# Performance work log

Measured on AMD Instinct MI355X. Metric: run time of the kernel, lower is better.

Reference implementation:

```python
import jax, jax.numpy as jnp
import numpy as np

B, S, D = 2, 2048, 2048
H, HKV = 16, 4
GROUPS = H // HKV
RQ, RKV = 1024, 512
DH, DR = 192, 64          # q_head_dim, rope dim
DN = DH - DR              # nrope dim = 128
DV = 128                  # v head dim
EPS = 1e-20


def setup_inputs() -> dict:
    key = jax.random.key(0)
    ks = jax.random.split(key, 8)
    inp = {
        "hidden_states": jax.random.normal(ks[0], (B, S, D), jnp.float32),
        # causal mask (0 = masked), as used by masked_fill(mask == 0, -inf)
        "attention_mask": jnp.tril(jnp.ones((S, S), jnp.int32))[None, None],
        "w_qa": jax.random.normal(ks[1], (D, RQ), jnp.float32) * 0.02,
        "b_qa": jnp.zeros((RQ,), jnp.float32),
        "g_q": jnp.ones((RQ,), jnp.float32),
        "w_qb": jax.random.normal(ks[2], (RQ, H * DH), jnp.float32) * 0.02,
        "b_qb": jnp.zeros((H * DH,), jnp.float32),
        "w_kva": jax.random.normal(ks[3], (D, RKV + DR), jnp.float32) * 0.02,
        "b_kva": jnp.zeros((RKV + DR,), jnp.float32),
        "g_kv": jnp.ones((RKV,), jnp.float32),
        "w_kvb": jax.random.normal(ks[4], (RKV, HKV * (DN + DV)), jnp.float32) * 0.02,
        "b_kvb": jnp.zeros((HKV * (DN + DV),), jnp.float32),
        "w_o": jax.random.normal(ks[5], (H * DV, D), jnp.float32) * 0.02,
        "b_o": jnp.zeros((D,), jnp.float32),
    }
    return inp


def _rmsnorm(x, g, eps=EPS):
    var = jnp.mean(x * x, axis=-1, keepdims=True)
    return x * jax.lax.rsqrt(var + eps) * g


def _rope_cos_sin(seq_len, dim, base=10000.0, dtype=jnp.float32):
    inv_freq = 1.0 / (base ** (jnp.arange(0, dim, 2, dtype=jnp.float32) / dim))
    t = jnp.arange(seq_len, dtype=jnp.float32)
    freqs = jnp.outer(t, inv_freq)                    # [S, dim/2]
    emb = jnp.concatenate([freqs, freqs], axis=-1)    # [S, dim]
    return jnp.cos(emb).astype(dtype), jnp.sin(emb).astype(dtype)


def _apply_rope(x, cos, sin):
    # x: [..., S, dr]; rotate_half convention
    d2 = x.shape[-1] // 2
    x1, x2 = x[..., :d2], x[..., d2:]
    rot = jnp.concatenate([-x2, x1], axis=-1)
    return x * cos + rot * sin


def reference(hidden_states, attention_mask, w_qa, b_qa, g_q, w_qb, b_qb,
              w_kva, b_kva, g_kv, w_kvb, b_kvb, w_o, b_o):
    b, s, _ = hidden_states.shape
    # --- Q: LoRA down -> RMSNorm -> LoRA up ---
    q_a = hidden_states @ w_qa + b_qa                         # [B,S,RQ]
    q_b = _rmsnorm(q_a, g_q) @ w_qb + b_qb                    # [B,S,H*DH]
    q_b = q_b.reshape(b, s, H, DH).transpose(0, 2, 1, 3)      # [B,H,S,DH]
    q_nrope, q_rope = q_b[..., :DN], q_b[..., DN:]
    # --- KV: LoRA down, split latent / shared rope key ---
    kv_a = hidden_states @ w_kva + b_kva                      # [B,S,RKV+DR]
    kv_c, k_rope = kv_a[..., :RKV], kv_a[..., RKV:]
    kv_b = _rmsnorm(kv_c, g_kv) @ w_kvb + b_kvb               # [B,S,HKV*(DN+DV)]
    kv_b = kv_b.reshape(b, s, HKV, DN + DV).transpose(0, 2, 1, 3)
    k_nrope, value_states = kv_b[..., :DN], kv_b[..., DN:]    # [B,HKV,S,DN/DV]
    # --- split RoPE ---
    cos, sin = _rope_cos_sin(s, DR, dtype=hidden_states.dtype)
    q_rope = _apply_rope(q_rope, cos, sin)                    # [B,H,S,DR]
    k_rope = _apply_rope(k_rope[:, None], cos, sin)           # [B,1,S,DR]
    # --- assemble heads (rope part first, matching source concat order) ---
    query_states = jnp.concatenate([q_rope, q_nrope], axis=-1)            # [B,H,S,DH]
    key_states = jnp.concatenate(
        [jnp.broadcast_to(k_rope, (b, HKV, s, DR)), k_nrope], axis=-1)    # [B,HKV,S,DH]
    # --- GQA expand kv heads ---
    key_states = jnp.repeat(key_states, GROUPS, axis=1)                   # [B,H,S,DH]
    value_states = jnp.repeat(value_states, GROUPS, axis=1)               # [B,H,S,DV]
    # --- attention ---
    scores = jnp.einsum('bhqd,bhkd->bhqk', query_states, key_states)
    scores = scores / jnp.sqrt(jnp.asarray(DH, scores.dtype))
    scores = jnp.where(attention_mask == 0, jnp.asarray(-1e9, scores.dtype), scores)
    weights = jax.nn.softmax(scores, axis=-1)
    attn_out = jnp.einsum('bhqk,bhkd->bhqd', weights, value_states)       # [B,H,S,DV]
    attn_out = attn_out.transpose(0, 2, 1, 3).reshape(b, s, H * DV)
    return attn_out @ w_o + b_o
```

## Files before the change

kernel.cpp:

```cpp
#include <hip/hip_runtime.h>
#include <hip/hip_bf16.h>
#include <stdint.h>

#define DEV static __device__ __forceinline__

typedef __attribute__((ext_vector_type(8))) short bf16x8;
typedef __attribute__((ext_vector_type(4))) float f32x4;
typedef __attribute__((ext_vector_type(16))) float f32x16;

constexpr int Bc = 2, Sc = 2048, Dc = 2048;
constexpr int Hc = 16, HKVc = 4;
constexpr int RQc = 1024, RKVc = 512;
constexpr int DHc = 192, DRc = 64, DVc = 128;

DEV unsigned short f2bf(float f) {
  union { float f; uint32_t u; } v; v.f = f;
  uint32_t r = v.u + 0x7FFFu + ((v.u >> 16) & 1u);
  return (unsigned short)(r >> 16);
}
DEV float bf2f(unsigned short u) {
  union { uint32_t u; float f; } v; v.u = ((uint32_t)u) << 16;
  return v.f;
}

DEV void gload_lds16(const unsigned short* g, unsigned short* l) {
  __builtin_amdgcn_global_load_lds(
      (const __attribute__((address_space(1))) unsigned int*)g,
      (__attribute__((address_space(3))) unsigned int*)l, 16, 0, 0);
}

__global__ void f2b_kernel(const float* __restrict__ in, unsigned short* __restrict__ out, int n) {
  int stride = gridDim.x * blockDim.x;
  for (int i = blockIdx.x * blockDim.x + threadIdx.x; i * 4 < n; i += stride) {
    float4 v = reinterpret_cast<const float4*>(in)[i];
    union { unsigned short u[4]; uint64_t q; } pk;
    pk.u[0] = f2bf(v.x); pk.u[1] = f2bf(v.y); pk.u[2] = f2bf(v.z); pk.u[3] = f2bf(v.w);
    reinterpret_cast<uint64_t*>(out)[i] = pk.q;
  }
}

__global__ void wtrans_kernel(const float* __restrict__ in, unsigned short* __restrict__ out,
                              int R, int C) {
  __shared__ float tile[32][33];
  const int c0 = blockIdx.x * 32, r0 = blockIdx.y * 32;
  const int tx = threadIdx.x & 31, ty = threadIdx.x >> 5;
#pragma unroll
  for (int i = 0; i < 32; i += 8)
    tile[ty + i][tx] = in[(size_t)(r0 + ty + i) * C + c0 + tx];
  __syncthreads();
#pragma unroll
  for (int i = 0; i < 32; i += 8)
    out[(size_t)(c0 + ty + i) * R + r0 + tx] = f2bf(tile[tx][ty + i]);
}

__global__ void rope_table_kernel(float* __restrict__ cosT, float* __restrict__ sinT) {
  int idx = blockIdx.x * blockDim.x + threadIdx.x;
  if (idx >= Sc * DRc) return;
  int t = idx >> 6;
  int j = idx & 63;
  float inv = exp2f(-13.287712379549449f * (float)(j & 31) * (1.0f / 32.0f));
  float f = (float)t * inv;
  cosT[idx] = cosf(f);
  sinT[idx] = sinf(f);
}

template<int R>
__global__ void rmsnorm_kernel(const float* __restrict__ in, int istride,
                               const float* __restrict__ g, unsigned short* __restrict__ out) {
  int row = blockIdx.x;
  const float* x = in + (size_t)row * istride;
  float ss = 0.f;
  for (int j = threadIdx.x; j < R; j += 256) { float v = x[j]; ss += v * v; }
  for (int off = 32; off; off >>= 1) ss += __shfl_down(ss, off, 64);
  __shared__ float wsum[4];
  if ((threadIdx.x & 63) == 0) wsum[threadIdx.x >> 6] = ss;
  __syncthreads();
  float tot = wsum[0] + wsum[1] + wsum[2] + wsum[3];
  float rs = rsqrtf(tot * (1.0f / R) + 1e-20f);
  for (int j = threadIdx.x; j < R; j += 256)
    out[(size_t)row * R + j] = f2bf(x[j] * rs * g[j]);
}

template<bool OUT_BF16, bool NG>
__global__ __launch_bounds__(256)
void gemm_tn_kernel(const unsigned short* __restrict__ A, const unsigned short* __restrict__ Bt,
                    const float* __restrict__ bias, void* __restrict__ Cout,
                    int M, int N, int K) {
  __shared__ __align__(16) unsigned short As[2][128 * 64];
  __shared__ __align__(16) unsigned short Bs[2][128 * 64];
  const int t = threadIdx.x, lane = t & 63, wave = t >> 6;
  const int wm = wave >> 1, wn = wave & 1;
  const int m0 = blockIdx.x * 128, n0 = blockIdx.y * 128;
  const int fr = lane & 15, fo = (lane >> 4) * 8, rg = lane >> 4;
  const int srow = lane >> 3;
  const int scol = (lane & 7) * 8;

  const unsigned short* Ap[4];
  const unsigned short* Bp[4];
#pragma unroll
  for (int i = 0; i < 4; ++i) {
    const int ar = m0 + wave * 32 + i * 8 + srow;
    Ap[i] = A + (size_t)ar * K + scol;
    int br = n0 + wave * 32 + i * 8 + srow;
    if (NG) br = br < N ? br : N - 1;
    Bp[i] = Bt + (size_t)br * K + scol;
  }

  auto stage = [&](int buf, int k0) {
#pragma unroll
    for (int i = 0; i < 4; ++i) {
      gload_lds16(Ap[i] + k0, &As[buf][(wave * 32 + i * 8) * 64]);
      gload_lds16(Bp[i] + k0, &Bs[buf][(wave * 32 + i * 8) * 64]);
    }
  };

  f32x4 acc[4][4] = {};
  const int nt = K >> 6;

  stage(0, 0);
  for (int tt = 0; tt < nt; ++tt) {
    const int cur = tt & 1;
    if (tt + 1 < nt) {
      stage(cur ^ 1, (tt + 1) * 64);
      asm volatile("s_waitcnt vmcnt(8)" ::: "memory");
    } else {
      asm volatile("s_waitcnt vmcnt(0)" ::: "memory");
    }
    __syncthreads();
#pragma unroll
    for (int kk = 0; kk < 64; kk += 32) {
      bf16x8 af[4], bf[4];
#pragma unroll
      for (int m = 0; m < 4; ++m)
        af[m] = *reinterpret_cast<const bf16x8*>(&As[cur][(wm * 64 + m * 16 + fr) * 64 + kk + fo]);
#pragma unroll
      for (int n = 0; n < 4; ++n)
        bf[n] = *reinterpret_cast<const bf16x8*>(&Bs[cur][(wn * 64 + n * 16 + fr) * 64 + kk + fo]);
      __builtin_amdgcn_s_setprio(1);
#pragma unroll
      for (int m = 0; m < 4; ++m)
#pragma unroll
        for (int n = 0; n < 4; ++n)
          acc[m][n] = __builtin_amdgcn_mfma_f32_16x16x32_bf16(af[m], bf[n], acc[m][n], 0, 0, 0);
      __builtin_amdgcn_s_setprio(0);
    }
    __syncthreads();
  }

#pragma unroll
  for (int m = 0; m < 4; ++m) {
    const int row = m0 + wm * 64 + m * 16 + rg * 4;
#pragma unroll
    for (int n = 0; n < 4; ++n) {
      const int col = n0 + wn * 64 + n * 16 + fr;
      if (NG && col >= N) continue;
      const float bb = bias[col];
#pragma unroll
      for (int r = 0; r < 4; ++r) {
        float v = acc[m][n][r] + bb;
        if (OUT_BF16)
          reinterpret_cast<unsigned short*>(Cout)[(size_t)(row + r) * N + col] = f2bf(v);
        else
          reinterpret_cast<float*>(Cout)[(size_t)(row + r) * N + col] = v;
      }
    }
  }
}

__global__ void prep_q_kernel(const unsigned short* __restrict__ qb,
                              const float* __restrict__ cosT, const float* __restrict__ sinT,
                              unsigned short* __restrict__ Q) {
  const float QS = 0.07216878364870323f * 1.4426950408889634f;
  int bs = blockIdx.x;
  int s = bs & (Sc - 1);
  int b = bs >> 11;
  int d = threadIdx.x;
  if (d >= 192) return;
  for (int h = 0; h < Hc; ++h) {
    const unsigned short* src = qb + (size_t)bs * (Hc * DHc) + h * DHc;
    float v;
    if (d < 128) {
      v = bf2f(src[d]);
    } else {
      int j = d - 128;
      float x = bf2f(src[128 + j]);
      float other = bf2f(src[128 + (j < 32 ? j + 32 : j - 32)]);
      float c = cosT[s * 64 + j], sn = sinT[s * 64 + j];
      v = (j < 32) ? (x * c - other * sn) : (x * c + other * sn);
    }
    Q[(((size_t)(b * Hc + h)) * Sc + s) * DHc + d] = f2bf(v * QS);
  }
}

__global__ void prep_k_kernel(const unsigned short* __restrict__ kvb,
                              const float* __restrict__ ccat,
                              const float* __restrict__ cosT, const float* __restrict__ sinT,
                              unsigned short* __restrict__ K) {
  int bs = blockIdx.x;
  int s = bs & (Sc - 1);
  int b = bs >> 11;
  int d = threadIdx.x;
  if (d >= 192) return;
  unsigned short ropeval = 0;
  if (d >= 128) {
    int j = d - 128;
    float x = ccat[(size_t)bs * 1600 + 1536 + j];
    float other = ccat[(size_t)bs * 1600 + 1536 + (j < 32 ? j + 32 : j - 32)];
    float c = cosT[s * 64 + j], sn = sinT[s * 64 + j];
    float v = (j < 32) ? (x * c - other * sn) : (x * c + other * sn);
    ropeval = f2bf(v);
  }
  const size_t off = (size_t)(s >> 6) * 12288 + (d >> 3) * 512 + (s & 63) * 8 + (d & 7);
  for (int kvh = 0; kvh < HKVc; ++kvh) {
    unsigned short o;
    if (d < 128) o = kvb[(size_t)bs * 1024 + kvh * 256 + d];
    else o = ropeval;
    K[(size_t)(b * HKVc + kvh) * Sc * DHc + off] = o;
  }
}

__global__ void vtrans_kernel(const unsigned short* __restrict__ kvb, unsigned short* __restrict__ Vt) {
  int idx = blockIdx.x;
  int dt = idx & 3;  idx >>= 2;
  int st = idx & 63; idx >>= 6;
  int kvh = idx & 3; idx >>= 2;
  int b = idx;
  __shared__ unsigned short tile[32][33];
  int t = threadIdx.x;
  int c = t & 31, r0 = t >> 5;
#pragma unroll
  for (int i = 0; i < 4; ++i) {
    int r = r0 + i * 8;
    int s = st * 32 + r;
    tile[r][c] = kvb[((size_t)(b * Sc + s)) * 1024 + kvh * 256 + 128 + dt * 32 + c];
  }
  __syncthreads();
#pragma unroll
  for (int i = 0; i < 4; ++i) {
    int r = r0 + i * 8;
    const int dd = dt * 32 + r;
    const int k = st * 32 + c;
    const size_t pos = (size_t)(k >> 6) * 8192 + ((k >> 3) & 7) * 1024 + dd * 8 + (k & 7);
    Vt[(size_t)((b * HKVc + kvh)) * DVc * Sc + pos] = tile[c][r];
  }
}

__global__ __launch_bounds__(128)
void attn_kernel(const unsigned short* __restrict__ Q, const unsigned short* __restrict__ Kt,
                 const unsigned short* __restrict__ Vt, unsigned short* __restrict__ attnOut) {
  __shared__ __align__(16) unsigned short Ks[2][12288];

  const int bid = blockIdx.x;
  const int g = bid & 7;
  const int b = g >> 2, kvh = g & 3;
  const int r2 = bid >> 3;
  const int hp = r2 & 1;
  const int u = r2 >> 1;
  const int w = threadIdx.x >> 6;
  const int h = kvh * 4 + hp * 2 + w;
  const int lane = threadIdx.x & 63;
  const int l31 = lane & 31, hi = lane >> 5;

  const unsigned short* Qh = Q + (size_t)(b * Hc + h) * Sc * DHc;
  const unsigned short* Kg = Kt + (size_t)(b * HKVc + kvh) * Sc * DHc;
  const unsigned short* Vg = Vt + (size_t)(b * HKVc + kvh) * DVc * Sc;

  auto stage = [&](int buf, int t) {
    const unsigned short* Kb = Kg + (size_t)t * 12288;
#pragma unroll
    for (int i = 0; i < 12; ++i) {
      const int ii = w * 12 + i;
      gload_lds16(Kb + ii * 512 + lane * 8, &Ks[buf][ii * 512]);
    }
  };

#pragma unroll 1
  for (int pan = 0; pan < 2; ++pan) {
    const int sub = pan ? u : (63 - u);
    const int q0 = sub * 32;
    const int q = q0 + l31;
    const int NT = (sub >> 1) + 1;

    bf16x8 qf[12];
#pragma unroll
    for (int f = 0; f < 12; ++f)
      qf[f] = *reinterpret_cast<const bf16x8*>(Qh + (size_t)q * DHc + f * 16 + hi * 8);

    f32x16 ot[4] = {};
    float m = -INFINITY, lsum = 0.f;

    auto half_step = [&](int cur, int tt, int halfsel, const bf16x8* vf, bool diag) {
      f32x16 s = {};
      const int r = halfsel * 32 + l31;
      __builtin_amdgcn_s_setprio(1);
#pragma unroll
      for (int f = 0; f < 12; ++f) {
        const int co = f * 2 + hi;
        bf16x8 kf = *reinterpret_cast<const bf16x8*>(&Ks[cur][co * 512 + r * 8]);
        s = __builtin_amdgcn_mfma_f32_32x32x16_bf16(kf, qf[f], s, 0, 0, 0);
      }
      __builtin_amdgcn_s_setprio(0);

      float v[16];
      if (diag) {
#pragma unroll
        for (int rr = 0; rr < 16; ++rr) {
          const int kl = (rr & 3) + 8 * (rr >> 2) + 4 * hi;
          v[rr] = (kl <= l31) ? s[rr] : -3.0e38f;
        }
      } else {
#pragma unroll
        for (int rr = 0; rr < 16; ++rr) v[rr] = s[rr];
      }

      float pmax = fmaxf(fmaxf(fmaxf(v[0], v[1]), fmaxf(v[2], v[3])),
                         fmaxf(fmaxf(v[4], v[5]), fmaxf(v[6], v[7])));
      float pmax2 = fmaxf(fmaxf(fmaxf(v[8], v[9]), fmaxf(v[10], v[11])),
                          fmaxf(fmaxf(v[12], v[13]), fmaxf(v[14], v[15])));
      pmax = fmaxf(pmax, pmax2);
      pmax = fmaxf(pmax, __shfl_xor(pmax, 32, 64));

      float cf = 1.f;
      if (!__all(pmax - m <= 8.0f)) {
        const float mnew = fmaxf(m, pmax);
        cf = exp2f(m - mnew);
        m = mnew;
#pragma unroll
        for (int dt = 0; dt < 4; ++dt)
#pragma unroll
          for (int rr = 0; rr < 16; ++rr) ot[dt][rr] *= cf;
      }

      float p[16];
      float rs = 0.f;
#pragma unroll
      for (int rr = 0; rr < 16; ++rr) { p[rr] = exp2f(v[rr] - m); rs += p[rr]; }
      rs += __shfl_xor(rs, 32, 64);
      lsum = lsum * cf + rs;

      uint32_t c[8], x[8];
#pragma unroll
      for (int i = 0; i < 8; ++i) {
        asm("v_cvt_pk_bf16_f32 %0, %1, %2" : "=v"(c[i]) : "v"(p[2 * i]), "v"(p[2 * i + 1]));
        x[i] = (uint32_t)__shfl_xor((int)c[i], 32, 64);
      }
      union { uint32_t w[4]; bf16x8 v8; } pa0, pa1;
      pa0.w[0] = hi ? x[2] : c[0];
      pa0.w[1] = hi ? x[3] : c[1];
      pa0.w[2] = hi ? c[2] : x[0];
      pa0.w[3] = hi ? c[3] : x[1];
      pa1.w[0] = hi ? x[6] : c[4];
      pa1.w[1] = hi ? x[7] : c[5];
      pa1.w[2] = hi ? c[6] : x[4];
      pa1.w[3] = hi ? c[7] : x[5];

      __builtin_amdgcn_s_setprio(1);
#pragma unroll
      for (int dt = 0; dt < 4; ++dt) {
        ot[dt] = __builtin_amdgcn_mfma_f32_32x32x16_bf16(vf[dt * 2], pa0.v8, ot[dt], 0, 0, 0);
        ot[dt] = __builtin_amdgcn_mfma_f32_32x32x16_bf16(vf[dt * 2 + 1], pa1.v8, ot[dt], 0, 0, 0);
      }
      __builtin_amdgcn_s_setprio(0);
      (void)tt;
    };

    stage(0, 0);
    asm volatile("s_waitcnt vmcnt(0)" ::: "memory");
    __syncthreads();

    for (int t = 0; t < NT; ++t) {
      const int cur = t & 1;
      const int kbase = t * 64;
      const bool act1 = (kbase + 32 <= q0);

      bf16x8 vf0[8];
#pragma unroll
      for (int dt = 0; dt < 4; ++dt)
#pragma unroll
        for (int k2 = 0; k2 < 2; ++k2) {
          const int c = k2 * 2 + hi;
          const int d = dt * 32 + l31;
          vf0[dt * 2 + k2] = *reinterpret_cast<const bf16x8*>(
              Vg + (size_t)t * 8192 + c * 1024 + d * 8);
        }
      __builtin_amdgcn_sched_barrier(0);
      if (t + 1 < NT) stage(cur ^ 1, t + 1);
      __builtin_amdgcn_sched_barrier(0);

      half_step(cur, t, 0, vf0, kbase == q0);

      if (act1) {
        bf16x8 vf1[8];
#pragma unroll
        for (int dt = 0; dt < 4; ++dt)
#pragma unroll
          for (int k2 = 0; k2 < 2; ++k2) {
            const int c = 4 + k2 * 2 + hi;
            const int d = dt * 32 + l31;
            vf1[dt * 2 + k2] = *reinterpret_cast<const bf16x8*>(
                Vg + (size_t)t * 8192 + c * 1024 + d * 8);
          }
        half_step(cur, t, 1, vf1, kbase + 32 == q0);
      }

      asm volatile("s_waitcnt vmcnt(0)" ::: "memory");
      __syncthreads();
    }

    const float inv = 1.0f / lsum;
    unsigned short* dst = attnOut + ((size_t)(b * Sc + q)) * (Hc * DVc) + h * DVc;
#pragma unroll
    for (int dt = 0; dt < 4; ++dt)
#pragma unroll
      for (int rq = 0; rq < 4; ++rq) {
        uint32_t lo = (uint32_t)f2bf(ot[dt][rq * 4 + 0] * inv) |
                      ((uint32_t)f2bf(ot[dt][rq * 4 + 1] * inv) << 16);
        uint32_t hi2 = (uint32_t)f2bf(ot[dt][rq * 4 + 2] * inv) |
                       ((uint32_t)f2bf(ot[dt][rq * 4 + 3] * inv) << 16);
        uint2 pk; pk.x = lo; pk.y = hi2;
        *reinterpret_cast<uint2*>(dst + dt * 32 + 8 * rq + 4 * hi) = pk;
      }
    __syncthreads();
  }
}

extern "C" void kernel_launch(void* const* d_in, const int* in_sizes, int n_in,
                              void* d_out, int out_size, void* d_ws, size_t ws_size,
                              hipStream_t stream) {
  (void)in_sizes; (void)n_in; (void)out_size; (void)ws_size;
  const float* hidden = (const float*)d_in[0];
  const float* w_qa  = (const float*)d_in[2];
  const float* b_qa  = (const float*)d_in[3];
  const float* g_q   = (const float*)d_in[4];
  const float* w_qb  = (const float*)d_in[5];
  const float* b_qb  = (const float*)d_in[6];
  const float* w_kva = (const float*)d_in[7];
  const float* b_kva = (const float*)d_in[8];
  const float* g_kv  = (const float*)d_in[9];
  const float* w_kvb = (const float*)d_in[10];
  const float* b_kvb = (const float*)d_in[11];
  const float* w_o   = (const float*)d_in[12];
  const float* b_o   = (const float*)d_in[13];
  float* out = (float*)d_out;

  char* ws = (char*)d_ws;
  size_t off = 0;
  auto alloc = [&](size_t bytes) -> void* {
    void* p = ws + off;
    off += (bytes + 255) & ~(size_t)255;
    return p;
  };
  const int MS = Bc * Sc;
  const int NCAT = RQc + RKVc + DRc;

  unsigned short* Xbf   = (unsigned short*)alloc((size_t)MS * Dc * 2);
  unsigned short* Wcat  = (unsigned short*)alloc((size_t)NCAT * Dc * 2);
  unsigned short* WqbT  = (unsigned short*)alloc((size_t)Hc * DHc * RQc * 2);
  unsigned short* WkvbT = (unsigned short*)alloc((size_t)HKVc * 256 * RKVc * 2);
  unsigned short* WoT   = (unsigned short*)alloc((size_t)Dc * Hc * DVc * 2);
  float* bcat = (float*)alloc((size_t)NCAT * 4);
  float* cosT = (float*)alloc((size_t)Sc * DRc * 4);
  float* sinT = (float*)alloc((size_t)Sc * DRc * 4);
  float* Ccat = (float*)alloc((size_t)MS * NCAT * 4);
  unsigned short* qan  = (unsigned short*)alloc((size_t)MS * RQc * 2);
  unsigned short* qb   = (unsigned short*)alloc((size_t)MS * Hc * DHc * 2);
  unsigned short* kvcn = (unsigned short*)alloc((size_t)MS * RKVc * 2);
  unsigned short* kvb  = (unsigned short*)alloc((size_t)MS * HKVc * 256 * 2);
  unsigned short* Qt   = (unsigned short*)alloc((size_t)Bc * Hc * Sc * DHc * 2);
  unsigned short* Kt   = (unsigned short*)alloc((size_t)Bc * HKVc * Sc * DHc * 2);
  unsigned short* Vt   = (unsigned short*)alloc((size_t)Bc * HKVc * DVc * Sc * 2);
  unsigned short* attnb= (unsigned short*)alloc((size_t)MS * Hc * DVc * 2);

  f2b_kernel<<<dim3(512), dim3(256), 0, stream>>>(hidden, Xbf, MS * Dc);
  wtrans_kernel<<<dim3(RQc / 32, Dc / 32), 256, 0, stream>>>(w_qa, Wcat, Dc, RQc);
  wtrans_kernel<<<dim3((RKVc + DRc) / 32, Dc / 32), 256, 0, stream>>>(w_kva, Wcat + (size_t)RQc * Dc, Dc, RKVc + DRc);
  wtrans_kernel<<<dim3(Hc * DHc / 32, RQc / 32), 256, 0, stream>>>(w_qb, WqbT, RQc, Hc * DHc);
  wtrans_kernel<<<dim3(HKVc * 256 / 32, RKVc / 32), 256, 0, stream>>>(w_kvb, WkvbT, RKVc, HKVc * 256);
  wtrans_kernel<<<dim3(Dc / 32, Hc * DVc / 32), 256, 0, stream>>>(w_o, WoT, Hc * DVc, Dc);
  hipMemcpyAsync(bcat, b_qa, (size_t)RQc * 4, hipMemcpyDeviceToDevice, stream);
  hipMemcpyAsync(bcat + RQc, b_kva, (size_t)(RKVc + DRc) * 4, hipMemcpyDeviceToDevice, stream);
  rope_table_kernel<<<dim3(512), dim3(256), 0, stream>>>(cosT, sinT);

  gemm_tn_kernel<false, true><<<dim3(MS / 128, (NCAT + 127) / 128), 256, 0, stream>>>(Xbf, Wcat, bcat, Ccat, MS, NCAT, Dc);
  rmsnorm_kernel<1024><<<dim3(MS), 256, 0, stream>>>(Ccat, NCAT, g_q, qan);
  rmsnorm_kernel<512><<<dim3(MS), 256, 0, stream>>>(Ccat + RQc, NCAT, g_kv, kvcn);
  gemm_tn_kernel<true, false><<<dim3(MS / 128, Hc * DHc / 128), 256, 0, stream>>>(qan, WqbT, b_qb, qb, MS, Hc * DHc, RQc);
  gemm_tn_kernel<true, false><<<dim3(MS / 128, HKVc * 256 / 128), 256, 0, stream>>>(kvcn, WkvbT, b_kvb, kvb, MS, HKVc * 256, RKVc);

  prep_q_kernel<<<dim3(MS), 256, 0, stream>>>(qb, cosT, sinT, Qt);
  prep_k_kernel<<<dim3(MS), 256, 0, stream>>>(kvb, Ccat, cosT, sinT, Kt);
  vtrans_kernel<<<dim3(Bc * HKVc * (Sc / 32) * (DVc / 32)), 256, 0, stream>>>(kvb, Vt);

  attn_kernel<<<dim3(512), dim3(128), 0, stream>>>(Qt, Kt, Vt, attnb);

  gemm_tn_kernel<false, false><<<dim3(MS / 128, Dc / 128), 256, 0, stream>>>(attnb, WoT, b_o, out, MS, Dc, Hc * DVc);
}
```

Baseline: 340.5 us.

## Process full 64-key tiles with one fused online-softmax step

For key tiles fully below the diagonal, the two 32-key QK^T MFMA chains are interleaved and a single online-softmax update (one max, one rescale, one row-sum) covers all 64 keys, followed by the PV MFMAs for both halves. Both halves of the V fragments are loaded up front for such tiles. Diagonal tiles keep the per-half path. This is meant to cut the softmax and reduction overhead per tile and give the scheduler independent MFMA chains to overlap. In exchange, register pressure rises from the extra scores and V fragments, which may reduce occupancy.

```diff
diff --git a/kernel.cpp b/kernel.cpp
--- a/kernel.cpp
+++ b/kernel.cpp
@@ -289,35 +289,20 @@
     f32x16 ot[4] = {};
     float m = -INFINITY, lsum = 0.f;
 
-    auto half_step = [&](int cur, int tt, int halfsel, const bf16x8* vf, bool diag) {
-      f32x16 s = {};
-      const int r = halfsel * 32 + l31;
-      __builtin_amdgcn_s_setprio(1);
-#pragma unroll
-      for (int f = 0; f < 12; ++f) {
-        const int co = f * 2 + hi;
-        bf16x8 kf = *reinterpret_cast<const bf16x8*>(&Ks[cur][co * 512 + r * 8]);
-        s = __builtin_amdgcn_mfma_f32_32x32x16_bf16(kf, qf[f], s, 0, 0, 0);
-      }
-      __builtin_amdgcn_s_setprio(0);
-
-      float v[16];
-      if (diag) {
-#pragma unroll
-        for (int rr = 0; rr < 16; ++rr) {
-          const int kl = (rr & 3) + 8 * (rr >> 2) + 4 * hi;
-          v[rr] = (kl <= l31) ? s[rr] : -3.0e38f;
-        }
-      } else {
-#pragma unroll
-        for (int rr = 0; rr < 16; ++rr) v[rr] = s[rr];
-      }
-
-      float pmax = fmaxf(fmaxf(fmaxf(v[0], v[1]), fmaxf(v[2], v[3])),
-                         fmaxf(fmaxf(v[4], v[5]), fmaxf(v[6], v[7])));
-      float pmax2 = fmaxf(fmaxf(fmaxf(v[8], v[9]), fmaxf(v[10], v[11])),
-                          fmaxf(fmaxf(v[12], v[13]), fmaxf(v[14], v[15])));
+    auto sm_pv = [&](const float* v0, const float* v1, const bf16x8* vf0, const bf16x8* vf1,
+                     bool both) {
+      float pmax = fmaxf(fmaxf(fmaxf(v0[0], v0[1]), fmaxf(v0[2], v0[3])),
+                         fmaxf(fmaxf(v0[4], v0[5]), fmaxf(v0[6], v0[7])));
+      float pmax2 = fmaxf(fmaxf(fmaxf(v0[8], v0[9]), fmaxf(v0[10], v0[11])),
+                          fmaxf(fmaxf(v0[12], v0[13]), fmaxf(v0[14], v0[15])));
       pmax = fmaxf(pmax, pmax2);
+      if (both) {
+        float pb = fmaxf(fmaxf(fmaxf(v1[0], v1[1]), fmaxf(v1[2], v1[3])),
+                         fmaxf(fmaxf(v1[4], v1[5]), fmaxf(v1[6], v1[7])));
+        float pb2 = fmaxf(fmaxf(fmaxf(v1[8], v1[9]), fmaxf(v1[10], v1[11])),
+                          fmaxf(fmaxf(v1[12], v1[13]), fmaxf(v1[14], v1[15])));
+        pmax = fmaxf(pmax, fmaxf(pb, pb2));
+      }
       pmax = fmaxf(pmax, __shfl_xor(pmax, 32, 64));
 
       float cf = 1.f;
@@ -331,20 +316,24 @@
           for (int rr = 0; rr < 16; ++rr) ot[dt][rr] *= cf;
       }
 
-      float p[16];
+      float p0[16], p1[16];
       float rs = 0.f;
 #pragma unroll
-      for (int rr = 0; rr < 16; ++rr) { p[rr] = exp2f(v[rr] - m); rs += p[rr]; }
+      for (int rr = 0; rr < 16; ++rr) { p0[rr] = exp2f(v0[rr] - m); rs += p0[rr]; }
+      if (both) {
+#pragma unroll
+        for (int rr = 0; rr < 16; ++rr) { p1[rr] = exp2f(v1[rr] - m); rs += p1[rr]; }
+      }
       rs += __shfl_xor(rs, 32, 64);
       lsum = lsum * cf + rs;
 
       uint32_t c[8], x[8];
 #pragma unroll
       for (int i = 0; i < 8; ++i) {
-        asm("v_cvt_pk_bf16_f32 %0, %1, %2" : "=v"(c[i]) : "v"(p[2 * i]), "v"(p[2 * i + 1]));
+        asm("v_cvt_pk_bf16_f32 %0, %1, %2" : "=v"(c[i]) : "v"(p0[2 * i]), "v"(p0[2 * i + 1]));
         x[i] = (uint32_t)__shfl_xor((int)c[i], 32, 64);
       }
-      union { uint32_t w[4]; bf16x8 v8; } pa0, pa1;
+      union { uint32_t w[4]; bf16x8 v8; } pa0, pa1, pb0, pb1;
       pa0.w[0] = hi ? x[2] : c[0];
       pa0.w[1] = hi ? x[3] : c[1];
       pa0.w[2] = hi ? c[2] : x[0];
@@ -353,15 +342,33 @@
       pa1.w[1] = hi ? x[7] : c[5];
       pa1.w[2] = hi ? c[6] : x[4];
       pa1.w[3] = hi ? c[7] : x[5];
+      if (both) {
+#pragma unroll
+        for (int i = 0; i < 8; ++i) {
+          asm("v_cvt_pk_bf16_f32 %0, %1, %2" : "=v"(c[i]) : "v"(p1[2 * i]), "v"(p1[2 * i + 1]));
+          x[i] = (uint32_t)__shfl_xor((int)c[i], 32, 64);
+        }
+        pb0.w[0] = hi ? x[2] : c[0];
+        pb0.w[1] = hi ? x[3] : c[1];
+        pb0.w[2] = hi ? c[2] : x[0];
+        pb0.w[3] = hi ? c[3] : x[1];
+        pb1.w[0] = hi ? x[6] : c[4];
+        pb1.w[1] = hi ? x[7] : c[5];
+        pb1.w[2] = hi ? c[6] : x[4];
+        pb1.w[3] = hi ? c[7] : x[5];
+      }
 
       __builtin_amdgcn_s_setprio(1);
 #pragma unroll
       for (int dt = 0; dt < 4; ++dt) {
-        ot[dt] = __builtin_amdgcn_mfma_f32_32x32x16_bf16(vf[dt * 2], pa0.v8, ot[dt], 0, 0, 0);
-        ot[dt] = __builtin_amdgcn_mfma_f32_32x32x16_bf16(vf[dt * 2 + 1], pa1.v8, ot[dt], 0, 0, 0);
+        ot[dt] = __builtin_amdgcn_mfma_f32_32x32x16_bf16(vf0[dt * 2], pa0.v8, ot[dt], 0, 0, 0);
+        ot[dt] = __builtin_amdgcn_mfma_f32_32x32x16_bf16(vf0[dt * 2 + 1], pa1.v8, ot[dt], 0, 0, 0);
+        if (both) {
+          ot[dt] = __builtin_amdgcn_mfma_f32_32x32x16_bf16(vf1[dt * 2], pb0.v8, ot[dt], 0, 0, 0);
+          ot[dt] = __builtin_amdgcn_mfma_f32_32x32x16_bf16(vf1[dt * 2 + 1], pb1.v8, ot[dt], 0, 0, 0);
+        }
       }
       __builtin_amdgcn_s_setprio(0);
-      (void)tt;
     };
 
     stage(0, 0);
@@ -371,36 +378,85 @@
     for (int t = 0; t < NT; ++t) {
       const int cur = t & 1;
       const int kbase = t * 64;
-      const bool act1 = (kbase + 32 <= q0);
-
-      bf16x8 vf0[8];
+      const bool full = (kbase + 32 < q0);
+
+      bf16x8 vf0[8], vf1[8];
 #pragma unroll
       for (int dt = 0; dt < 4; ++dt)
 #pragma unroll
         for (int k2 = 0; k2 < 2; ++k2) {
-          const int c = k2 * 2 + hi;
           const int d = dt * 32 + l31;
           vf0[dt * 2 + k2] = *reinterpret_cast<const bf16x8*>(
-              Vg + (size_t)t * 8192 + c * 1024 + d * 8);
+              Vg + (size_t)t * 8192 + (k2 * 2 + hi) * 1024 + d * 8);
         }
+      if (full) {
+#pragma unroll
+        for (int dt = 0; dt < 4; ++dt)
+#pragma unroll
+          for (int k2 = 0; k2 < 2; ++k2) {
+            const int d = dt * 32 + l31;
+            vf1[dt * 2 + k2] = *reinterpret_cast<const bf16x8*>(
+                Vg + (size_t)t * 8192 + (4 + k2 * 2 + hi) * 1024 + d * 8);
+          }
+      }
       __builtin_amdgcn_sched_barrier(0);
       if (t + 1 < NT) stage(cur ^ 1, t + 1);
       __builtin_amdgcn_sched_barrier(0);
 
-      half_step(cur, t, 0, vf0, kbase == q0);
-
-      if (act1) {
-        bf16x8 vf1[8];
-#pragma unroll
-        for (int dt = 0; dt < 4; ++dt)
-#pragma unroll
-          for (int k2 = 0; k2 < 2; ++k2) {
-            const int c = 4 + k2 * 2 + hi;
-            const int d = dt * 32 + l31;
-            vf1[dt * 2 + k2] = *reinterpret_cast<const bf16x8*>(
-                Vg + (size_t)t * 8192 + c * 1024 + d * 8);
+      if (full) {
+        f32x16 sa = {}, sb = {};
+        __builtin_amdgcn_s_setprio(1);
+#pragma unroll
+        for (int f = 0; f < 12; ++f) {
+          const int co = f * 2 + hi;
+          bf16x8 kf0 = *reinterpret_cast<const bf16x8*>(&Ks[cur][co * 512 + l31 * 8]);
+          bf16x8 kf1 = *reinterpret_cast<const bf16x8*>(&Ks[cur][co * 512 + (32 + l31) * 8]);
+          sa = __builtin_amdgcn_mfma_f32_32x32x16_bf16(kf0, qf[f], sa, 0, 0, 0);
+          sb = __builtin_amdgcn_mfma_f32_32x32x16_bf16(kf1, qf[f], sb, 0, 0, 0);
+        }
+        __builtin_amdgcn_s_setprio(0);
+        float v0[16], v1[16];
+#pragma unroll
+        for (int rr = 0; rr < 16; ++rr) { v0[rr] = sa[rr]; v1[rr] = sb[rr]; }
+        sm_pv(v0, v1, vf0, vf1, true);
+      } else {
+#pragma unroll 1
+        for (int halfsel = 0; halfsel < 2; ++halfsel) {
+          const int ks = kbase + halfsel * 32;
+          if (ks > q0) break;
+          f32x16 s = {};
+          const int r = halfsel * 32 + l31;
+          __builtin_amdgcn_s_setprio(1);
+#pragma unroll
+          for (int f = 0; f < 12; ++f) {
+            const int co = f * 2 + hi;
+            bf16x8 kf = *reinterpret_cast<const bf16x8*>(&Ks[cur][co * 512 + r * 8]);
+            s = __builtin_amdgcn_mfma_f32_32x32x16_bf16(kf, qf[f], s, 0, 0, 0);
           }
-        half_step(cur, t, 1, vf1, kbase + 32 == q0);
+          __builtin_amdgcn_s_setprio(0);
+          float v[16];
+          if (ks == q0) {
+#pragma unroll
+            for (int rr = 0; rr < 16; ++rr) {
+              const int kl = (rr & 3) + 8 * (rr >> 2) + 4 * hi;
+              v[rr] = (kl <= l31) ? s[rr] : -3.0e38f;
+            }
+          } else {
+#pragma unroll
+            for (int rr = 0; rr < 16; ++rr) v[rr] = s[rr];
+          }
+          sm_pv(v, nullptr, halfsel ? vf1 : vf0, nullptr, false);
+          if (!halfsel && kbase + 32 <= q0) {
+#pragma unroll
+            for (int dt = 0; dt < 4; ++dt)
+#pragma unroll
+              for (int k2 = 0; k2 < 2; ++k2) {
+                const int d = dt * 32 + l31;
+                vf1[dt * 2 + k2] = *reinterpret_cast<const bf16x8*>(
+                    Vg + (size_t)t * 8192 + (4 + k2 * 2 + hi) * 1024 + d * 8);
+              }
+          }
+        }
       }
 
       asm volatile("s_waitcnt vmcnt(0)" ::: "memory");
```

Result: slower. 351.1 us (+3.1%).

## Split attention KV range across two waves per head and merge partial softmax

Applied to the files above, without the earlier changes.

Attention blocks now use four waves, with two waves per head that each handle alternating 32-key sub-tiles. At the end the two partial softmax states are merged through shared memory. The K and V layouts are repacked into 32-row tiles to match. This aims to double wave-level parallelism and shorten the serial KV loop per wave. In exchange it adds an LDS reduction, extra syncs, a larger block, and idle waves on odd-length diagonal tiles.

```diff
diff --git a/kernel.cpp b/kernel.cpp
--- a/kernel.cpp
+++ b/kernel.cpp
@@ -210,7 +210,7 @@
     float v = (j < 32) ? (x * c - other * sn) : (x * c + other * sn);
     ropeval = f2bf(v);
   }
-  const size_t off = (size_t)(s >> 6) * 12288 + (d >> 3) * 512 + (s & 63) * 8 + (d & 7);
+  const size_t off = (size_t)(s >> 5) * 6144 + (d >> 3) * 256 + (s & 31) * 8 + (d & 7);
   for (int kvh = 0; kvh < HKVc; ++kvh) {
     unsigned short o;
     if (d < 128) o = kvb[(size_t)bs * 1024 + kvh * 256 + d];
@@ -240,24 +240,27 @@
     int r = r0 + i * 8;
     const int dd = dt * 32 + r;
     const int k = st * 32 + c;
-    const size_t pos = (size_t)(k >> 6) * 8192 + ((k >> 3) & 7) * 1024 + dd * 8 + (k & 7);
+    const size_t pos = (size_t)(k >> 5) * 4096 + ((k >> 3) & 3) * 1024 + dd * 8 + (k & 7);
     Vt[(size_t)((b * HKVc + kvh)) * DVc * Sc + pos] = tile[c][r];
   }
 }
 
-__global__ __launch_bounds__(128)
+__global__ __launch_bounds__(256)
 void attn_kernel(const unsigned short* __restrict__ Q, const unsigned short* __restrict__ Kt,
                  const unsigned short* __restrict__ Vt, unsigned short* __restrict__ attnOut) {
-  __shared__ __align__(16) unsigned short Ks[2][12288];
+  __shared__ __align__(16) unsigned short Ks[4][6144];
+  __shared__ float mlS[4][2][32];
 
   const int bid = blockIdx.x;
   const int g = bid & 7;
   const int b = g >> 2, kvh = g & 3;
-  const int r2 = bid >> 3;
-  const int hp = r2 & 1;
-  const int u = r2 >> 1;
+  const int rr = bid >> 3;
+  const int hp = rr & 1;
+  const int u = rr >> 1;
   const int w = threadIdx.x >> 6;
-  const int h = kvh * 4 + hp * 2 + w;
+  const int hd = w >> 1;
+  const int sp = w & 1;
+  const int h = kvh * 4 + hp * 2 + hd;
   const int lane = threadIdx.x & 63;
   const int l31 = lane & 31, hi = lane >> 5;
 
@@ -265,13 +268,12 @@
   const unsigned short* Kg = Kt + (size_t)(b * HKVc + kvh) * Sc * DHc;
   const unsigned short* Vg = Vt + (size_t)(b * HKVc + kvh) * DVc * Sc;
 
-  auto stage = [&](int buf, int t) {
-    const unsigned short* Kb = Kg + (size_t)t * 12288;
-#pragma unroll
-    for (int i = 0; i < 12; ++i) {
-      const int ii = w * 12 + i;
-      gload_lds16(Kb + ii * 512 + lane * 8, &Ks[buf][ii * 512]);
-    }
+  auto stage = [&](int i) {
+    const unsigned short* src = Kg + (size_t)i * 12288;
+    unsigned short* dst = &Ks[(i & 1) * 2][0];
+#pragma unroll
+    for (int j = 0; j < 6; ++j)
+      gload_lds16(src + j * 2048 + threadIdx.x * 8, dst + j * 2048 + threadIdx.x * 8);
   };
 
 #pragma unroll 1
@@ -279,7 +281,7 @@
     const int sub = pan ? u : (63 - u);
     const int q0 = sub * 32;
     const int q = q0 + l31;
-    const int NT = (sub >> 1) + 1;
+    const int NS = (sub >> 1) + 1;
 
     bf16x8 qf[12];
 #pragma unroll
@@ -289,137 +291,148 @@
     f32x16 ot[4] = {};
     float m = -INFINITY, lsum = 0.f;
 
-    auto half_step = [&](int cur, int tt, int halfsel, const bf16x8* vf, bool diag) {
-      f32x16 s = {};
-      const int r = halfsel * 32 + l31;
-      __builtin_amdgcn_s_setprio(1);
-#pragma unroll
-      for (int f = 0; f < 12; ++f) {
-        const int co = f * 2 + hi;
-        bf16x8 kf = *reinterpret_cast<const bf16x8*>(&Ks[cur][co * 512 + r * 8]);
-        s = __builtin_amdgcn_mfma_f32_32x32x16_bf16(kf, qf[f], s, 0, 0, 0);
-      }
-      __builtin_amdgcn_s_setprio(0);
-
-      float v[16];
-      if (diag) {
-#pragma unroll
-        for (int rr = 0; rr < 16; ++rr) {
-          const int kl = (rr & 3) + 8 * (rr >> 2) + 4 * hi;
-          v[rr] = (kl <= l31) ? s[rr] : -3.0e38f;
-        }
-      } else {
-#pragma unroll
-        for (int rr = 0; rr < 16; ++rr) v[rr] = s[rr];
-      }
-
-      float pmax = fmaxf(fmaxf(fmaxf(v[0], v[1]), fmaxf(v[2], v[3])),
-                         fmaxf(fmaxf(v[4], v[5]), fmaxf(v[6], v[7])));
-      float pmax2 = fmaxf(fmaxf(fmaxf(v[8], v[9]), fmaxf(v[10], v[11])),
-                          fmaxf(fmaxf(v[12], v[13]), fmaxf(v[14], v[15])));
-      pmax = fmaxf(pmax, pmax2);
-      pmax = fmaxf(pmax, __shfl_xor(pmax, 32, 64));
-
-      float cf = 1.f;
-      if (!__all(pmax - m <= 8.0f)) {
-        const float mnew = fmaxf(m, pmax);
-        cf = exp2f(m - mnew);
-        m = mnew;
-#pragma unroll
-        for (int dt = 0; dt < 4; ++dt)
-#pragma unroll
-          for (int rr = 0; rr < 16; ++rr) ot[dt][rr] *= cf;
-      }
-
-      float p[16];
-      float rs = 0.f;
-#pragma unroll
-      for (int rr = 0; rr < 16; ++rr) { p[rr] = exp2f(v[rr] - m); rs += p[rr]; }
-      rs += __shfl_xor(rs, 32, 64);
-      lsum = lsum * cf + rs;
-
-      uint32_t c[8], x[8];
-#pragma unroll
-      for (int i = 0; i < 8; ++i) {
-        asm("v_cvt_pk_bf16_f32 %0, %1, %2" : "=v"(c[i]) : "v"(p[2 * i]), "v"(p[2 * i + 1]));
-        x[i] = (uint32_t)__shfl_xor((int)c[i], 32, 64);
-      }
-      union { uint32_t w[4]; bf16x8 v8; } pa0, pa1;
-      pa0.w[0] = hi ? x[2] : c[0];
-      pa0.w[1] = hi ? x[3] : c[1];
-      pa0.w[2] = hi ? c[2] : x[0];
-      pa0.w[3] = hi ? c[3] : x[1];
-      pa1.w[0] = hi ? x[6] : c[4];
-      pa1.w[1] = hi ? x[7] : c[5];
-      pa1.w[2] = hi ? c[6] : x[4];
-      pa1.w[3] = hi ? c[7] : x[5];
-
-      __builtin_amdgcn_s_setprio(1);
-#pragma unroll
-      for (int dt = 0; dt < 4; ++dt) {
-        ot[dt] = __builtin_amdgcn_mfma_f32_32x32x16_bf16(vf[dt * 2], pa0.v8, ot[dt], 0, 0, 0);
-        ot[dt] = __builtin_amdgcn_mfma_f32_32x32x16_bf16(vf[dt * 2 + 1], pa1.v8, ot[dt], 0, 0, 0);
-      }
-      __builtin_amdgcn_s_setprio(0);
-      (void)tt;
-    };
-
-    stage(0, 0);
+    stage(0);
     asm volatile("s_waitcnt vmcnt(0)" ::: "memory");
     __syncthreads();
 
-    for (int t = 0; t < NT; ++t) {
-      const int cur = t & 1;
-      const int kbase = t * 64;
-      const bool act1 = (kbase + 32 <= q0);
-
-      bf16x8 vf0[8];
-#pragma unroll
-      for (int dt = 0; dt < 4; ++dt)
-#pragma unroll
-        for (int k2 = 0; k2 < 2; ++k2) {
-          const int c = k2 * 2 + hi;
-          const int d = dt * 32 + l31;
-          vf0[dt * 2 + k2] = *reinterpret_cast<const bf16x8*>(
-              Vg + (size_t)t * 8192 + c * 1024 + d * 8);
-        }
+    for (int i = 0; i < NS; ++i) {
+      const int t = 2 * i + sp;
+      const bool active = (t <= sub);
+      const int p = i & 1;
+
+      bf16x8 vf[8];
+      if (active) {
+#pragma unroll
+        for (int dt = 0; dt < 4; ++dt)
+#pragma unroll
+          for (int k2 = 0; k2 < 2; ++k2)
+            vf[dt * 2 + k2] = *reinterpret_cast<const bf16x8*>(
+                Vg + (size_t)t * 4096 + (k2 * 2 + hi) * 1024 + (dt * 32 + l31) * 8);
+      }
       __builtin_amdgcn_sched_barrier(0);
-      if (t + 1 < NT) stage(cur ^ 1, t + 1);
+      if (i + 1 < NS) stage(i + 1);
       __builtin_amdgcn_sched_barrier(0);
 
-      half_step(cur, t, 0, vf0, kbase == q0);
-
-      if (act1) {
-        bf16x8 vf1[8];
-#pragma unroll
-        for (int dt = 0; dt < 4; ++dt)
-#pragma unroll
-          for (int k2 = 0; k2 < 2; ++k2) {
-            const int c = 4 + k2 * 2 + hi;
-            const int d = dt * 32 + l31;
-            vf1[dt * 2 + k2] = *reinterpret_cast<const bf16x8*>(
-                Vg + (size_t)t * 8192 + c * 1024 + d * 8);
+      if (active) {
+        const unsigned short* kb = &Ks[p * 2 + sp][0];
+        f32x16 s = {};
+        __builtin_amdgcn_s_setprio(1);
+#pragma unroll
+        for (int f = 0; f < 12; ++f) {
+          bf16x8 kf = *reinterpret_cast<const bf16x8*>(kb + (f * 2 + hi) * 256 + l31 * 8);
+          s = __builtin_amdgcn_mfma_f32_32x32x16_bf16(kf, qf[f], s, 0, 0, 0);
+        }
+        __builtin_amdgcn_s_setprio(0);
+
+        float v[16];
+        if (t == sub) {
+#pragma unroll
+          for (int rrr = 0; rrr < 16; ++rrr) {
+            const int kl = (rrr & 3) + 8 * (rrr >> 2) + 4 * hi;
+            v[rrr] = (kl <= l31) ? s[rrr] : -3.0e38f;
           }
-        half_step(cur, t, 1, vf1, kbase + 32 == q0);
+        } else {
+#pragma unroll
+          for (int rrr = 0; rrr < 16; ++rrr) v[rrr] = s[rrr];
+        }
+
+        float pmax = fmaxf(fmaxf(fmaxf(v[0], v[1]), fmaxf(v[2], v[3])),
+                           fmaxf(fmaxf(v[4], v[5]), fmaxf(v[6], v[7])));
+        float pmax2 = fmaxf(fmaxf(fmaxf(v[8], v[9]), fmaxf(v[10], v[11])),
+                            fmaxf(fmaxf(v[12], v[13]), fmaxf(v[14], v[15])));
+        pmax = fmaxf(pmax, pmax2);
+        pmax = fmaxf(pmax, __shfl_xor(pmax, 32, 64));
+
+        float cf = 1.f;
+        if (!__all(pmax - m <= 8.0f)) {
+          const float mnew = fmaxf(m, pmax);
+          cf = exp2f(m - mnew);
+          m = mnew;
+#pragma unroll
+          for (int dt = 0; dt < 4; ++dt)
+#pragma unroll
+            for (int rrr = 0; rrr < 16; ++rrr) ot[dt][rrr] *= cf;
+        }
+
+        float pp[16];
+        float rs = 0.f;
+#pragma unroll
+        for (int rrr = 0; rrr < 16; ++rrr) { pp[rrr] = exp2f(v[rrr] - m); rs += pp[rrr]; }
+        rs += __shfl_xor(rs, 32, 64);
+        lsum = lsum * cf + rs;
+
+        uint32_t c[8], x[8];
+#pragma unroll
+        for (int ii = 0; ii < 8; ++ii) {
+          asm("v_cvt_pk_bf16_f32 %0, %1, %2" : "=v"(c[ii]) : "v"(pp[2 * ii]), "v"(pp[2 * ii + 1]));
+          x[ii] = (uint32_t)__shfl_xor((int)c[ii], 32, 64);
+        }
+        union { uint32_t w[4]; bf16x8 v8; } pa0, pa1;
+        pa0.w[0] = hi ? x[2] : c[0];
+        pa0.w[1] = hi ? x[3] : c[1];
+        pa0.w[2] = hi ? c[2] : x[0];
+        pa0.w[3] = hi ? c[3] : x[1];
+        pa1.w[0] = hi ? x[6] : c[4];
+        pa1.w[1] = hi ? x[7] : c[5];
+        pa1.w[2] = hi ? c[6] : x[4];
+        pa1.w[3] = hi ? c[7] : x[5];
+
+        __builtin_amdgcn_s_setprio(1);
+#pragma unroll
+        for (int dt = 0; dt < 4; ++dt) {
+          ot[dt] = __builtin_amdgcn_mfma_f32_32x32x16_bf16(vf[dt * 2], pa0.v8, ot[dt], 0, 0, 0);
+          ot[dt] = __builtin_amdgcn_mfma_f32_32x32x16_bf16(vf[dt * 2 + 1], pa1.v8, ot[dt], 0, 0, 0);
+        }
+        __builtin_amdgcn_s_setprio(0);
       }
 
       asm volatile("s_waitcnt vmcnt(0)" ::: "memory");
       __syncthreads();
     }
 
-    const float inv = 1.0f / lsum;
-    unsigned short* dst = attnOut + ((size_t)(b * Sc + q)) * (Hc * DVc) + h * DVc;
-#pragma unroll
-    for (int dt = 0; dt < 4; ++dt)
-#pragma unroll
-      for (int rq = 0; rq < 4; ++rq) {
-        uint32_t lo = (uint32_t)f2bf(ot[dt][rq * 4 + 0] * inv) |
-                      ((uint32_t)f2bf(ot[dt][rq * 4 + 1] * inv) << 16);
-        uint32_t hi2 = (uint32_t)f2bf(ot[dt][rq * 4 + 2] * inv) |
-                       ((uint32_t)f2bf(ot[dt][rq * 4 + 3] * inv) << 16);
-        uint2 pk; pk.x = lo; pk.y = hi2;
-        *reinterpret_cast<uint2*>(dst + dt * 32 + 8 * rq + 4 * hi) = pk;
-      }
+    if (hi == 0) { mlS[w][0][l31] = m; mlS[w][1][l31] = lsum; }
+    __syncthreads();
+    const int pw = w ^ 1;
+    const float mp = mlS[pw][0][l31];
+    const float lp = mlS[pw][1][l31];
+    const float mstar = fmaxf(m, mp);
+    const float sc = exp2f(m - mstar);
+    const float lstar = lsum * sc + lp * exp2f(mp - mstar);
+    float* LO = (float*)&Ks[0][0];
+
+    if (sp == 1) {
+#pragma unroll
+      for (int dt = 0; dt < 4; ++dt)
+#pragma unroll
+        for (int rq = 0; rq < 4; ++rq) {
+          float4 vv;
+          vv.x = ot[dt][rq * 4 + 0] * sc;
+          vv.y = ot[dt][rq * 4 + 1] * sc;
+          vv.z = ot[dt][rq * 4 + 2] * sc;
+          vv.w = ot[dt][rq * 4 + 3] * sc;
+          *reinterpret_cast<float4*>(&LO[(size_t)(hd * 32 + l31) * 132 + dt * 32 + 8 * rq + 4 * hi]) = vv;
+        }
+    }
+    __syncthreads();
+    if (sp == 0) {
+      const float inv = 1.0f / lstar;
+      unsigned short* dst = attnOut + ((size_t)(b * Sc + q)) * (Hc * DVc) + h * DVc;
+#pragma unroll
+      for (int dt = 0; dt < 4; ++dt)
+#pragma unroll
+        for (int rq = 0; rq < 4; ++rq) {
+          float4 pv = *reinterpret_cast<const float4*>(
+              &LO[(size_t)(hd * 32 + l31) * 132 + dt * 32 + 8 * rq + 4 * hi]);
+          const float o0 = (ot[dt][rq * 4 + 0] * sc + pv.x) * inv;
+          const float o1 = (ot[dt][rq * 4 + 1] * sc + pv.y) * inv;
+          const float o2 = (ot[dt][rq * 4 + 2] * sc + pv.z) * inv;
+          const float o3 = (ot[dt][rq * 4 + 3] * sc + pv.w) * inv;
+          uint2 pk;
+          pk.x = (uint32_t)f2bf(o0) | ((uint32_t)f2bf(o1) << 16);
+          pk.y = (uint32_t)f2bf(o2) | ((uint32_t)f2bf(o3) << 16);
+          *reinterpret_cast<uint2*>(dst + dt * 32 + 8 * rq + 4 * hi) = pk;
+        }
+    }
     __syncthreads();
   }
 }
@@ -491,7 +504,7 @@
   prep_k_kernel<<<dim3(MS), 256, 0, stream>>>(kvb, Ccat, cosT, sinT, Kt);
   vtrans_kernel<<<dim3(Bc * HKVc * (Sc / 32) * (DVc / 32)), 256, 0, stream>>>(kvb, Vt);
 
-  attn_kernel<<<dim3(512), dim3(128), 0, stream>>>(Qt, Kt, Vt, attnb);
+  attn_kernel<<<dim3(512), dim3(256), 0, stream>>>(Qt, Kt, Vt, attnb);
 
   gemm_tn_kernel<false, false><<<dim3(MS / 128, Dc / 128), 256, 0, stream>>>(attnb, WoT, b_o, out, MS, Dc, Hc * DVc);
 }
```

Result: slower. 365.1 us (+7.2%).
